# Kernel optimization log

Measured on AMD Instinct MI355X. Metric: run time of the kernel, lower is better.

The kernel has to match this reference:

```python
import jax, jax.numpy as jnp
import numpy as np

B, S, N = 8, 32, 64
F_NODE = 32
TRI = N * (N - 1) // 2        # 2016 upper-triangular edge features per step
DIN = F_NODE + TRI            # 2048 GATConv input dim (node feats + broadcast edge feats)
H, DOUT = 4, 256              # num_heads, hidden_channels
R = 1024                      # rnn_hidden_size
OUT = TRI                     # edge_in_channels * N*(N-1)/2


def setup_inputs() -> dict:
    key = jax.random.key(0)
    ks = jax.random.split(key, 16)
    def nrm(k, shape, fan):
        return jax.random.normal(k, shape, jnp.float32) / np.float32(np.sqrt(fan))
    # complete directed graph (no self loops; GATConv adds them)
    idx = np.arange(N)
    src = np.repeat(idx, N); dst = np.tile(idx, N)
    keep = src != dst
    edge_index = jnp.asarray(np.stack([src[keep], dst[keep]]), dtype=jnp.int32)  # [2, 4032]
    return {
        "x_node": jax.random.normal(ks[0], (B, S, N, F_NODE), jnp.float32),
        "x_edge": jax.random.normal(ks[1], (B, S, TRI), jnp.float32),
        "edge_index": edge_index,
        "W_gat": nrm(ks[2], (DIN, H * DOUT), DIN),
        "att_src": nrm(ks[3], (H, DOUT), DOUT),
        "att_dst": nrm(ks[4], (H, DOUT), DOUT),
        "b_gat": jnp.zeros((DOUT,), jnp.float32),
        "W_ih0": nrm(ks[5], (3 * R, N * DOUT), N * DOUT),
        "W_hh0": nrm(ks[6], (3 * R, R), R),
        "b_ih0": jnp.zeros((3 * R,), jnp.float32),
        "b_hh0": jnp.zeros((3 * R,), jnp.float32),
        "W_ih1": nrm(ks[7], (3 * R, R), R),
        "W_hh1": nrm(ks[8], (3 * R, R), R),
        "b_ih1": jnp.zeros((3 * R,), jnp.float32),
        "b_hh1": jnp.zeros((3 * R,), jnp.float32),
        "W_fc": nrm(ks[9], (R, OUT), R),
        "b_fc": jnp.zeros((OUT,), jnp.float32),
    }


def _gru_layer(x, Wih, Whh, bih, bhh):
    # x: [B, S, D] -> [B, S, R], PyTorch GRU equations
    def step(h, xt):
        gi = xt @ Wih.T + bih
        gh = h @ Whh.T + bhh
        i_r, i_z, i_n = jnp.split(gi, 3, axis=-1)
        h_r, h_z, h_n = jnp.split(gh, 3, axis=-1)
        r = jax.nn.sigmoid(i_r + h_r)
        z = jax.nn.sigmoid(i_z + h_z)
        n = jnp.tanh(i_n + r * h_n)
        h = (1.0 - z) * n + z * h
        return h, h
    h0 = jnp.zeros((x.shape[0], Whh.shape[1]), x.dtype)
    _, ys = jax.lax.scan(step, h0, jnp.swapaxes(x, 0, 1))
    return jnp.swapaxes(ys, 0, 1)


def reference(x_node, x_edge, edge_index, W_gat, att_src, att_dst, b_gat,
              W_ih0, W_hh0, b_ih0, b_hh0, W_ih1, W_hh1, b_ih1, b_hh1, W_fc, b_fc):
    # concat node feats with per-step edge features broadcast to every node
    x = jnp.concatenate(
        [x_node, jnp.broadcast_to(x_edge[:, :, None, :], (B, S, N, TRI))], axis=-1)
    xg = x.reshape(B * S, N, DIN)                         # batch all (b,t) graphs
    h = (xg @ W_gat).reshape(B * S, N, H, DOUT)           # per-head projections
    a_s = jnp.einsum('bnhe,he->bnh', h, att_src)
    a_d = jnp.einsum('bnhe,he->bnh', h, att_dst)
    # edge (src j -> dst i): leaky_relu(a_src[j] + a_dst[i]); dense over [dst, src]
    scores = jax.nn.leaky_relu(a_d[:, :, None, :] + a_s[:, None, :, :], 0.2)  # [BS, i, j, H]
    adj = jnp.zeros((N, N), bool).at[edge_index[1], edge_index[0]].set(True)
    adj = adj.at[jnp.arange(N), jnp.arange(N)].set(True)  # GATConv add_self_loops=True
    scores = jnp.where(adj[None, :, :, None], scores, -jnp.inf)
    alpha = jax.nn.softmax(scores, axis=2)                # softmax over source neighbors
    gat = jnp.einsum('bish,bshe->bihe', alpha, h).mean(axis=2) + b_gat  # concat=False -> head mean
    gat = jax.nn.relu(gat)                                # [BS, N, DOUT]
    seq = gat.reshape(B, S, N * DOUT)
    y = _gru_layer(seq, W_ih0, W_hh0, b_ih0, b_hh0)
    y = _gru_layer(y, W_ih1, W_hh1, b_ih1, b_hh1)
    return y[:, -1] @ W_fc + b_fc                         # [B, OUT]
```

## Files before the change

kernel.cpp:

```cpp
#include <hip/hip_runtime.h>
#include <hip/hip_bf16.h>

using bf16 = __hip_bfloat16;
typedef __bf16 bf16x8 __attribute__((ext_vector_type(8)));
typedef float f32x4 __attribute__((ext_vector_type(4)));


__device__ __forceinline__ void unp2(unsigned int u, float& a, float& b) {
  a = __uint_as_float(u << 16);
  b = __uint_as_float(u & 0xffff0000u);
}

__device__ __forceinline__ bf16x8 cvt8(float4 a, float4 b) {
  bf16x8 r;
  r[0] = (__bf16)a.x; r[1] = (__bf16)a.y; r[2] = (__bf16)a.z; r[3] = (__bf16)a.w;
  r[4] = (__bf16)b.x; r[5] = (__bf16)b.y; r[6] = (__bf16)b.z; r[7] = (__bf16)b.w;
  return r;
}

__global__ __launch_bounds__(256) void gru_fused_k(
    const float* __restrict__ X0,
    const float* __restrict__ Whh0,
    const float* __restrict__ bhh0,
    float* __restrict__ y0,
    const float* __restrict__ Wih1,
    const float* __restrict__ bih1,
    const float* __restrict__ Whh1,
    const float* __restrict__ bhh1,
    float* __restrict__ y1,
    int t) {
  __shared__ float sA[8][1024];
  __shared__ float sB[8][1024];
  const int tid = threadIdx.x;
  const int wv = tid >> 6, lane = tid & 63;

  if (blockIdx.x < 256) {
    if (t >= 32) return;
    const int s = t;
    if (s == 0) {
#pragma unroll
      for (int q = 0; q < 8; ++q) {
        int idx = q * 256 + tid;
        *(float4*)&sA[idx >> 8][(idx & 255) * 4] = make_float4(0.f, 0.f, 0.f, 0.f);
      }
    } else {
#pragma unroll
      for (int q = 0; q < 8; ++q) {
        int idx = q * 256 + tid;
        int b = idx >> 8, kf = (idx & 255) * 4;
        *(float4*)&sA[b][kf] =
            *(const float4*)&y0[(size_t)(b * 32 + s - 1) * 1024 + kf];
      }
    }
    __syncthreads();
    const int j = blockIdx.x * 4 + wv;
    const float* Wr = Whh0 + (size_t)j * 1024;
    const float* Wz = Whh0 + (size_t)(1024 + j) * 1024;
    const float* Wn = Whh0 + (size_t)(2048 + j) * 1024;
    float accR[8] = {}, accZ[8] = {}, accN[8] = {};
#pragma unroll
    for (int kk = 0; kk < 4; ++kk) {
      const int k = kk * 256 + lane * 4;
      float4 wr = *(const float4*)&Wr[k];
      float4 wz = *(const float4*)&Wz[k];
      float4 wn = *(const float4*)&Wn[k];
#pragma unroll
      for (int b = 0; b < 8; ++b) {
        float4 h4 = *(const float4*)&sA[b][k];
        accR[b] += h4.x * wr.x + h4.y * wr.y + h4.z * wr.z + h4.w * wr.w;
        accZ[b] += h4.x * wz.x + h4.y * wz.y + h4.z * wz.z + h4.w * wz.w;
        accN[b] += h4.x * wn.x + h4.y * wn.y + h4.z * wn.z + h4.w * wn.w;
      }
    }
#pragma unroll
    for (int d = 1; d < 64; d <<= 1) {
#pragma unroll
      for (int b = 0; b < 8; ++b) {
        accR[b] += __shfl_xor(accR[b], d);
        accZ[b] += __shfl_xor(accZ[b], d);
        accN[b] += __shfl_xor(accN[b], d);
      }
    }
    if (lane < 8) {
      const int b = lane;
      float sr = 0.f, sz = 0.f, sn = 0.f;
#pragma unroll
      for (int bb = 0; bb < 8; ++bb)
        if (b == bb) { sr = accR[bb]; sz = accZ[bb]; sn = accN[bb]; }
      const float* gip = X0 + (size_t)(b * 32 + s) * 3072;
      float r = 1.0f / (1.0f + __expf(-(gip[j] + sr + bhh0[j])));
      float z = 1.0f / (1.0f + __expf(-(gip[1024 + j] + sz + bhh0[1024 + j])));
      float n = tanhf(gip[2048 + j] + r * (sn + bhh0[2048 + j]));
      float hp = sA[b][j];
      y0[(size_t)(b * 32 + s) * 1024 + j] = (1.0f - z) * n + z * hp;
    }
  } else {
    if (t < 1) return;
    const int s = t - 1;
    {
#pragma unroll
      for (int q = 0; q < 8; ++q) {
        int idx = q * 256 + tid;
        int b = idx >> 8, kf = (idx & 255) * 4;
        *(float4*)&sA[b][kf] =
            *(const float4*)&y0[(size_t)(b * 32 + s) * 1024 + kf];
        float4 v = make_float4(0.f, 0.f, 0.f, 0.f);
        if (s > 0)
          v = *(const float4*)&y1[(size_t)(b * 32 + s - 1) * 1024 + kf];
        *(float4*)&sB[b][kf] = v;
      }
    }
    __syncthreads();
    const int j = (blockIdx.x - 256) * 4 + wv;
    const float* WiR = Wih1 + (size_t)j * 1024;
    const float* WiZ = Wih1 + (size_t)(1024 + j) * 1024;
    const float* WiN = Wih1 + (size_t)(2048 + j) * 1024;
    const float* WhR = Whh1 + (size_t)j * 1024;
    const float* WhZ = Whh1 + (size_t)(1024 + j) * 1024;
    const float* WhN = Whh1 + (size_t)(2048 + j) * 1024;
    float accRZ[8] = {}, accZZ[8] = {}, accIN[8] = {}, accHN[8] = {};
#pragma unroll
    for (int kk = 0; kk < 4; ++kk) {
      const int k = kk * 256 + lane * 4;
      float4 wir = *(const float4*)&WiR[k];
      float4 wiz = *(const float4*)&WiZ[k];
      float4 win = *(const float4*)&WiN[k];
      float4 whr = *(const float4*)&WhR[k];
      float4 whz = *(const float4*)&WhZ[k];
      float4 whn = *(const float4*)&WhN[k];
#pragma unroll
      for (int b = 0; b < 8; ++b) {
        float4 x4 = *(const float4*)&sA[b][k];
        float4 h4 = *(const float4*)&sB[b][k];
        accRZ[b] += x4.x * wir.x + x4.y * wir.y + x4.z * wir.z + x4.w * wir.w
                  + h4.x * whr.x + h4.y * whr.y + h4.z * whr.z + h4.w * whr.w;
        accZZ[b] += x4.x * wiz.x + x4.y * wiz.y + x4.z * wiz.z + x4.w * wiz.w
                  + h4.x * whz.x + h4.y * whz.y + h4.z * whz.z + h4.w * whz.w;
        accIN[b] += x4.x * win.x + x4.y * win.y + x4.z * win.z + x4.w * win.w;
        accHN[b] += h4.x * whn.x + h4.y * whn.y + h4.z * whn.z + h4.w * whn.w;
      }
    }
#pragma unroll
    for (int d = 1; d < 64; d <<= 1) {
#pragma unroll
      for (int b = 0; b < 8; ++b) {
        accRZ[b] += __shfl_xor(accRZ[b], d);
        accZZ[b] += __shfl_xor(accZZ[b], d);
        accIN[b] += __shfl_xor(accIN[b], d);
        accHN[b] += __shfl_xor(accHN[b], d);
      }
    }
    if (lane < 8) {
      const int b = lane;
      float srz = 0.f, szz = 0.f, sin_ = 0.f, shn = 0.f;
#pragma unroll
      for (int bb = 0; bb < 8; ++bb)
        if (b == bb) { srz = accRZ[bb]; szz = accZZ[bb]; sin_ = accIN[bb]; shn = accHN[bb]; }
      float r = 1.0f / (1.0f + __expf(-(srz + bih1[j] + bhh1[j])));
      float z = 1.0f / (1.0f + __expf(-(szz + bih1[1024 + j] + bhh1[1024 + j])));
      float n = tanhf(sin_ + bih1[2048 + j] + r * (shn + bhh1[2048 + j]));
      float hp = sB[b][j];
      y1[(size_t)(b * 32 + s) * 1024 + j] = (1.0f - z) * n + z * hp;
    }
  }
}

__global__ __launch_bounds__(256) void gemm_bt16_k(const __bf16* __restrict__ A,
                                                   const float* __restrict__ Bm,
                                                   float* __restrict__ Cp,
                                                   int N, int K, int ksper) {
  __shared__ __bf16 As[256][40];
  __shared__ __bf16 Bs[128][40];
  const int tid = threadIdx.x;
  const int bn = blockIdx.x * 128;
  const int lane = tid & 63, wv = tid >> 6;
  const int wr = wv >> 1, wc = wv & 1;
  const int lr = lane & 15, kh = lane >> 4;
  const int brow = tid >> 1, bhalf = tid & 1;
  f32x4 acc[8][4] = {};
  const int kstot = K >> 5;
  int ks0 = blockIdx.z * ksper;
  int ks1 = ks0 + ksper; if (ks1 > kstot) ks1 = kstot;
  uint4 ra0, ra1, ra2, ra3; float4 rb0, rb1, rb2, rb3;
  {
    const int k0 = ks0 << 5;
    const uint4* ap = (const uint4*)(A + (size_t)tid * K + k0);
    ra0 = ap[0]; ra1 = ap[1]; ra2 = ap[2]; ra3 = ap[3];
    const float* bp = Bm + (size_t)(bn + brow) * K + k0 + bhalf * 16;
    rb0 = ((const float4*)bp)[0]; rb1 = ((const float4*)bp)[1];
    rb2 = ((const float4*)bp)[2]; rb3 = ((const float4*)bp)[3];
  }
  for (int ks = ks0; ks < ks1; ++ks) {
    __syncthreads();
    *(uint4*)&As[tid][0]  = ra0;
    *(uint4*)&As[tid][8]  = ra1;
    *(uint4*)&As[tid][16] = ra2;
    *(uint4*)&As[tid][24] = ra3;
    *(bf16x8*)&Bs[brow][bhalf * 16] = cvt8(rb0, rb1);
    *(bf16x8*)&Bs[brow][bhalf * 16 + 8] = cvt8(rb2, rb3);
    __syncthreads();
    if (ks + 1 < ks1) {
      const int k0 = (ks + 1) << 5;
      const uint4* ap = (const uint4*)(A + (size_t)tid * K + k0);
      ra0 = ap[0]; ra1 = ap[1]; ra2 = ap[2]; ra3 = ap[3];
      const float* bp = Bm + (size_t)(bn + brow) * K + k0 + bhalf * 16;
      rb0 = ((const float4*)bp)[0]; rb1 = ((const float4*)bp)[1];
      rb2 = ((const float4*)bp)[2]; rb3 = ((const float4*)bp)[3];
    }
    bf16x8 bfv[4];
#pragma unroll
    for (int ni = 0; ni < 4; ++ni)
      bfv[ni] = *(const bf16x8*)&Bs[wc * 64 + ni * 16 + lr][kh * 8];
#pragma unroll
    for (int mi = 0; mi < 8; ++mi) {
      bf16x8 af = *(const bf16x8*)&As[wr * 128 + mi * 16 + lr][kh * 8];
#pragma unroll
      for (int ni = 0; ni < 4; ++ni)
        acc[mi][ni] = __builtin_amdgcn_mfma_f32_16x16x32_bf16(af, bfv[ni],
                                                              acc[mi][ni], 0, 0, 0);
    }
  }
  float* cp = Cp + (size_t)blockIdx.z * 256 * N;
#pragma unroll
  for (int mi = 0; mi < 8; ++mi) {
#pragma unroll
    for (int ni = 0; ni < 4; ++ni) {
      const int row = wr * 128 + mi * 16 + kh * 4;
      const int col = bn + wc * 64 + ni * 16 + lr;
#pragma unroll
      for (int j = 0; j < 4; ++j)
        cp[(size_t)(row + j) * N + col] = acc[mi][ni][j];
    }
  }
}

template <bool BT>
__global__ __launch_bounds__(256) void mfma_gemm_k(const float* __restrict__ A,
                                                   const float* __restrict__ Bm,
                                                   float* __restrict__ Cp,
                                                   int M, int N, int K,
                                                   int lda, int ldb, int ksper) {
  __shared__ __bf16 As[128][40];
  __shared__ __bf16 Bs[128][40];
  const int tid = threadIdx.x;
  const int bm = blockIdx.y * 128, bn = blockIdx.x * 128;
  const int lane = tid & 63, wv = tid >> 6;
  const int wr = wv >> 1, wc = wv & 1;
  const int lr = lane & 15, kh = lane >> 4;
  f32x4 acc[4][4] = {};
  const int kstot = K >> 5;
  int ks0 = blockIdx.z * ksper;
  int ks1 = ks0 + ksper; if (ks1 > kstot) ks1 = kstot;
  for (int ks = ks0; ks < ks1; ++ks) {
    const int k0 = ks << 5;
    __syncthreads();
    {
      const int row = tid >> 1, half = tid & 1;
      const float* ap = A + (size_t)(bm + row) * lda + k0 + half * 16;
      float4 f0 = ((const float4*)ap)[0], f1 = ((const float4*)ap)[1];
      float4 f2 = ((const float4*)ap)[2], f3 = ((const float4*)ap)[3];
      *(bf16x8*)&As[row][half * 16] = cvt8(f0, f1);
      *(bf16x8*)&As[row][half * 16 + 8] = cvt8(f2, f3);
    }
    if (BT) {
      const int row = tid >> 1, half = tid & 1;
      const float* bp = Bm + (size_t)(bn + row) * ldb + k0 + half * 16;
      float4 f0 = ((const float4*)bp)[0], f1 = ((const float4*)bp)[1];
      float4 f2 = ((const float4*)bp)[2], f3 = ((const float4*)bp)[3];
      *(bf16x8*)&Bs[row][half * 16] = cvt8(f0, f1);
      *(bf16x8*)&Bs[row][half * 16 + 8] = cvt8(f2, f3);
    } else {
      const int kk = tid >> 3, ng = tid & 7;
      const float* bp = Bm + (size_t)(k0 + kk) * ldb + bn + ng * 16;
      float4 f[4];
#pragma unroll
      for (int q = 0; q < 4; ++q) f[q] = ((const float4*)bp)[q];
#pragma unroll
      for (int q = 0; q < 4; ++q) {
        Bs[ng * 16 + q * 4 + 0][kk] = (__bf16)f[q].x;
        Bs[ng * 16 + q * 4 + 1][kk] = (__bf16)f[q].y;
        Bs[ng * 16 + q * 4 + 2][kk] = (__bf16)f[q].z;
        Bs[ng * 16 + q * 4 + 3][kk] = (__bf16)f[q].w;
      }
    }
    __syncthreads();
    bf16x8 af[4], bfv[4];
#pragma unroll
    for (int mi = 0; mi < 4; ++mi)
      af[mi] = *(const bf16x8*)&As[wr * 64 + mi * 16 + lr][kh * 8];
#pragma unroll
    for (int ni = 0; ni < 4; ++ni)
      bfv[ni] = *(const bf16x8*)&Bs[wc * 64 + ni * 16 + lr][kh * 8];
#pragma unroll
    for (int mi = 0; mi < 4; ++mi)
#pragma unroll
      for (int ni = 0; ni < 4; ++ni)
        acc[mi][ni] = __builtin_amdgcn_mfma_f32_16x16x32_bf16(af[mi], bfv[ni],
                                                              acc[mi][ni], 0, 0, 0);
  }
  float* cp = Cp + (size_t)blockIdx.z * M * N;
#pragma unroll
  for (int mi = 0; mi < 4; ++mi) {
#pragma unroll
    for (int ni = 0; ni < 4; ++ni) {
      const int row = bm + wr * 64 + mi * 16 + kh * 4;
      const int col = bn + wc * 64 + ni * 16 + lr;
#pragma unroll
      for (int j = 0; j < 4; ++j)
        cp[(size_t)(row + j) * N + col] = acc[mi][ni][j];
    }
  }
}

__global__ __launch_bounds__(256) void reduce_k(const float* __restrict__ Cp,
                                                const float* __restrict__ bias,
                                                float* __restrict__ C,
                                                int MN, int N, int nsk) {
  int i = (blockIdx.x * 256 + threadIdx.x) * 4;
  if (i >= MN) return;
  float4 s = make_float4(0.f, 0.f, 0.f, 0.f);
  if (bias) s = *(const float4*)&bias[i % N];
  for (int sk = 0; sk < nsk; ++sk) {
    float4 p = *(const float4*)&Cp[(size_t)sk * MN + i];
    s.x += p.x; s.y += p.y; s.z += p.z; s.w += p.w;
  }
  *(float4*)&C[i] = s;
}

__global__ __launch_bounds__(256) void node_h_k(const float* __restrict__ xn,
                                                const float* __restrict__ Wg,
                                                const float* __restrict__ he,
                                                bf16* __restrict__ hbuf) {
  __shared__ float xns[64][32];
  __shared__ float wgs[32][256];
  const int cq = blockIdx.x, g = blockIdx.y;
  const int tid = threadIdx.x;
  for (int idx = tid; idx < 2048; idx += 256) xns[idx >> 5][idx & 31] = xn[g * 2048 + idx];
  for (int r = 0; r < 32; ++r) wgs[r][tid] = Wg[r * 1024 + cq * 256 + tid];
  __syncthreads();
  const float hev = he[g * 1024 + cq * 256 + tid];
  for (int n0 = 0; n0 < 64; n0 += 8) {
    float acc[8];
#pragma unroll
    for (int nn = 0; nn < 8; ++nn) acc[nn] = hev;
    for (int f = 0; f < 32; ++f) {
      float w = wgs[f][tid];
#pragma unroll
      for (int nn = 0; nn < 8; ++nn) acc[nn] += xns[n0 + nn][f] * w;
    }
#pragma unroll
    for (int nn = 0; nn < 8; ++nn)
      hbuf[(size_t)(g * 64 + n0 + nn) * 1024 + cq * 256 + tid] = __float2bfloat16(acc[nn]);
  }
}

__global__ __launch_bounds__(256) void as_ad_k(const bf16* __restrict__ hbuf,
                                               const float* __restrict__ att_s,
                                               const float* __restrict__ att_d,
                                               float* __restrict__ as_o,
                                               float* __restrict__ ad_o) {
  const int tid = threadIdx.x;
  const int lane = tid & 63, wv = tid >> 6;
  const int row = blockIdx.x * 4 + wv;
  const int hd = lane >> 4;
  const int e0 = (lane & 15) * 16;
  float as_r[16], ad_r[16];
#pragma unroll
  for (int q = 0; q < 4; ++q) {
    float4 v = *(const float4*)(att_s + hd * 256 + e0 + q * 4);
    as_r[q * 4 + 0] = v.x; as_r[q * 4 + 1] = v.y; as_r[q * 4 + 2] = v.z; as_r[q * 4 + 3] = v.w;
    float4 w = *(const float4*)(att_d + hd * 256 + e0 + q * 4);
    ad_r[q * 4 + 0] = w.x; ad_r[q * 4 + 1] = w.y; ad_r[q * 4 + 2] = w.z; ad_r[q * 4 + 3] = w.w;
  }
  const uint4* hp = (const uint4*)(hbuf + (size_t)row * 1024 + lane * 16);
  uint4 p0 = hp[0], p1 = hp[1];
  float hv[16];
  unp2(p0.x, hv[0], hv[1]);  unp2(p0.y, hv[2], hv[3]);
  unp2(p0.z, hv[4], hv[5]);  unp2(p0.w, hv[6], hv[7]);
  unp2(p1.x, hv[8], hv[9]);  unp2(p1.y, hv[10], hv[11]);
  unp2(p1.z, hv[12], hv[13]); unp2(p1.w, hv[14], hv[15]);
  float ps = 0.f, pd = 0.f;
#pragma unroll
  for (int i = 0; i < 16; ++i) { ps += as_r[i] * hv[i]; pd += ad_r[i] * hv[i]; }
#pragma unroll
  for (int m = 1; m < 16; m <<= 1) { ps += __shfl_xor(ps, m); pd += __shfl_xor(pd, m); }
  if ((lane & 15) == 0) { as_o[row * 4 + hd] = ps; ad_o[row * 4 + hd] = pd; }
}

__global__ __launch_bounds__(256) void attn_agg_k(const bf16* __restrict__ hbuf,
                                                  const float* __restrict__ as_i,
                                                  const float* __restrict__ ad_i,
                                                  const float* __restrict__ bgat,
                                                  __bf16* __restrict__ seq) {
  __shared__ float ass[256], ads[256], bgs[256];
  __shared__ float alpha[4][64][64];
  __shared__ float hq[64][260];
  const int g = blockIdx.x, tid = threadIdx.x;
  ass[tid] = as_i[g * 256 + tid];
  ads[tid] = ad_i[g * 256 + tid];
  bgs[tid] = bgat[tid];
  __syncthreads();
  {
    const int hd = tid >> 6, i = tid & 63;
    const float ad = ads[i * 4 + hd];
    float m = -1e30f;
    for (int j = 0; j < 64; ++j) {
      float s = ad + ass[j * 4 + hd];
      s = s > 0.0f ? s : 0.2f * s;
      m = fmaxf(m, s);
    }
    float sum = 0.0f;
    for (int j = 0; j < 64; ++j) {
      float s = ad + ass[j * 4 + hd];
      s = s > 0.0f ? s : 0.2f * s;
      sum += __expf(s - m);
    }
    const float inv = 1.0f / sum;
    for (int j = 0; j < 64; ++j) {
      float s = ad + ass[j * 4 + hd];
      s = s > 0.0f ? s : 0.2f * s;
      alpha[hd][j][i] = __expf(s - m) * inv;
    }
  }
  const int i = tid & 63, eq = tid >> 6;
  float acc[64] = {};
  for (int hd = 0; hd < 4; ++hd) {
    __syncthreads();
    for (int idx = tid; idx < 2048; idx += 256) {
      int j = idx >> 5, ch = idx & 31;
      uint4 p = *(const uint4*)(hbuf + (size_t)(g * 64 + j) * 1024 + hd * 256 + ch * 8);
      float f0, f1, f2, f3, f4, f5, f6, f7;
      unp2(p.x, f0, f1); unp2(p.y, f2, f3); unp2(p.z, f4, f5); unp2(p.w, f6, f7);
      *(float4*)&hq[j][ch * 8] = make_float4(f0, f1, f2, f3);
      *(float4*)&hq[j][ch * 8 + 4] = make_float4(f4, f5, f6, f7);
    }
    __syncthreads();
    for (int j = 0; j < 64; ++j) {
      const float a = alpha[hd][j][i];
      const float* hr = &hq[j][eq * 64];
#pragma unroll
      for (int q = 0; q < 16; ++q) {
        float4 hv = *(const float4*)(hr + q * 4);
        acc[q * 4 + 0] += a * hv.x; acc[q * 4 + 1] += a * hv.y;
        acc[q * 4 + 2] += a * hv.z; acc[q * 4 + 3] += a * hv.w;
      }
    }
  }
  __bf16* op = seq + (size_t)g * 16384 + i * 256 + eq * 64;
#pragma unroll
  for (int q = 0; q < 8; ++q) {
    float4 lo, hi;
    lo.x = fmaxf(bgs[eq * 64 + q * 8 + 0] + 0.25f * acc[q * 8 + 0], 0.0f);
    lo.y = fmaxf(bgs[eq * 64 + q * 8 + 1] + 0.25f * acc[q * 8 + 1], 0.0f);
    lo.z = fmaxf(bgs[eq * 64 + q * 8 + 2] + 0.25f * acc[q * 8 + 2], 0.0f);
    lo.w = fmaxf(bgs[eq * 64 + q * 8 + 3] + 0.25f * acc[q * 8 + 3], 0.0f);
    hi.x = fmaxf(bgs[eq * 64 + q * 8 + 4] + 0.25f * acc[q * 8 + 4], 0.0f);
    hi.y = fmaxf(bgs[eq * 64 + q * 8 + 5] + 0.25f * acc[q * 8 + 5], 0.0f);
    hi.z = fmaxf(bgs[eq * 64 + q * 8 + 6] + 0.25f * acc[q * 8 + 6], 0.0f);
    hi.w = fmaxf(bgs[eq * 64 + q * 8 + 7] + 0.25f * acc[q * 8 + 7], 0.0f);
    *(bf16x8*)(op + q * 8) = cvt8(lo, hi);
  }
}

__global__ __launch_bounds__(256) void fc_k(const float* __restrict__ y1,
                                            const float* __restrict__ Wfc,
                                            const float* __restrict__ bfc,
                                            float* __restrict__ out) {
  __shared__ float As[8][1024];
  const int tid = threadIdx.x;
  for (int idx = tid; idx < 8192; idx += 256) {
    int b = idx >> 10, k = idx & 1023;
    As[b][k] = y1[(size_t)(b * 32 + 31) * 1024 + k];
  }
  __syncthreads();
  const int ol = tid >> 2, kq = tid & 3;
  const int o = blockIdx.x * 64 + ol;
  float acc[8] = {};
  if (o < 2016) {
    for (int i2 = 0; i2 < 256; ++i2) {
      int k = i2 * 4 + kq;
      float w = Wfc[(size_t)k * 2016 + o];
#pragma unroll
      for (int b = 0; b < 8; ++b) acc[b] += As[b][k] * w;
    }
  }
#pragma unroll
  for (int b = 0; b < 8; ++b) {
    acc[b] += __shfl_xor(acc[b], 1);
    acc[b] += __shfl_xor(acc[b], 2);
  }
  if (kq == 0 && o < 2016) {
#pragma unroll
    for (int b = 0; b < 8; ++b) out[b * 2016 + o] = acc[b] + bfc[o];
  }
}

extern "C" void kernel_launch(void* const* d_in, const int* in_sizes, int n_in,
                              void* d_out, int out_size, void* d_ws, size_t ws_size,
                              hipStream_t stream) {
  (void)in_sizes; (void)n_in; (void)out_size; (void)ws_size;
  const float* x_node = (const float*)d_in[0];
  const float* x_edge = (const float*)d_in[1];
  const float* W_gat = (const float*)d_in[3];
  const float* att_s = (const float*)d_in[4];
  const float* att_d = (const float*)d_in[5];
  const float* b_gat = (const float*)d_in[6];
  const float* W_ih0 = (const float*)d_in[7];
  const float* W_hh0 = (const float*)d_in[8];
  const float* b_ih0 = (const float*)d_in[9];
  const float* b_hh0 = (const float*)d_in[10];
  const float* W_ih1 = (const float*)d_in[11];
  const float* W_hh1 = (const float*)d_in[12];
  const float* b_ih1 = (const float*)d_in[13];
  const float* b_hh1 = (const float*)d_in[14];
  const float* W_fc  = (const float*)d_in[15];
  const float* b_fc  = (const float*)d_in[16];

  char* ws = (char*)d_ws;
  size_t off = 0;
  float*  he  = (float*)(ws + off);  off += 256u * 1024 * 4;
  float*  a_s = (float*)(ws + off);  off += 256u * 64 * 4 * 4;
  float*  a_d = (float*)(ws + off);  off += 256u * 64 * 4 * 4;
  bf16*   hb  = (bf16*)(ws + off);   off += 256u * 64 * 1024 * 2;
  __bf16* seq = (__bf16*)(ws + off); off += 256u * 16384 * 2;
  float*  X0  = (float*)(ws + off);  off += 256u * 3072 * 4;
  float*  y0  = (float*)(ws + off);  off += 256u * 1024 * 4;
  float*  y1  = (float*)(ws + off);  off += 256u * 1024 * 4;
  off = (off + 255) & ~(size_t)255;
  float*  Cp  = (float*)(ws + off);  off += (size_t)16 * 256 * 3072 * 4;

  mfma_gemm_k<false><<<dim3(8, 2, 8), 256, 0, stream>>>(
      x_edge, W_gat + 32 * 1024, Cp, 256, 1024, 2016, 2016, 1024, 8);
  reduce_k<<<256, 256, 0, stream>>>(Cp, nullptr, he, 256 * 1024, 1024, 8);
  node_h_k<<<dim3(4, 256), 256, 0, stream>>>(x_node, W_gat, he, hb);
  as_ad_k<<<4096, 256, 0, stream>>>(hb, att_s, att_d, a_s, a_d);
  attn_agg_k<<<256, 256, 0, stream>>>(hb, a_s, a_d, b_gat, seq);
  gemm_bt16_k<<<dim3(24, 1, 16), 256, 0, stream>>>(seq, W_ih0, Cp,
                                                   3072, 16384, 32);
  reduce_k<<<768, 256, 0, stream>>>(Cp, b_ih0, X0, 256 * 3072, 3072, 16);
  for (int t = 0; t <= 32; ++t)
    gru_fused_k<<<512, 256, 0, stream>>>(X0, W_hh0, b_hh0, y0,
                                         W_ih1, b_ih1, W_hh1, b_hh1, y1, t);
  fc_k<<<32, 256, 0, stream>>>(y1, W_fc, b_fc, (float*)d_out);
}
```

Baseline: 765.4 us.

## Store GRU recurrent weights in bf16 and split layer-1 work across more blocks

Adds a kernel that converts W_hh0, W_ih1 and W_hh1 to bf16 once per call, which halves the weight bytes each GRU step streams from memory. The layer-1 part of the fused GRU kernel now runs on twice as many blocks. Each block handles two output units, with separate waves for the input and hidden projections, and their partial sums are combined through shared memory. This raises parallelism for the weight-bandwidth-bound recurrent steps. In exchange it adds a conversion pass over 3x3M weights, lowers weight precision, and reads the previous h directly from global memory instead of staging it in LDS.

```diff
diff --git a/kernel.cpp b/kernel.cpp
--- a/kernel.cpp
+++ b/kernel.cpp
@@ -18,19 +18,34 @@
   return r;
 }
 
-__global__ __launch_bounds__(256) void gru_fused_k(
+__global__ __launch_bounds__(256) void wcvt_k(const float* __restrict__ a,
+                                              const float* __restrict__ b,
+                                              const float* __restrict__ c,
+                                              __bf16* __restrict__ A,
+                                              __bf16* __restrict__ B,
+                                              __bf16* __restrict__ C) {
+  const int i = (blockIdx.x * 256 + threadIdx.x) * 8;
+  float4 x0 = *(const float4*)&a[i], x1 = *(const float4*)&a[i + 4];
+  *(bf16x8*)&A[i] = cvt8(x0, x1);
+  float4 y0_ = *(const float4*)&b[i], y1_ = *(const float4*)&b[i + 4];
+  *(bf16x8*)&B[i] = cvt8(y0_, y1_);
+  float4 z0 = *(const float4*)&c[i], z1 = *(const float4*)&c[i + 4];
+  *(bf16x8*)&C[i] = cvt8(z0, z1);
+}
+
+__global__ __launch_bounds__(256) void gru_fused2_k(
     const float* __restrict__ X0,
-    const float* __restrict__ Whh0,
+    const __bf16* __restrict__ Wb0,
     const float* __restrict__ bhh0,
     float* __restrict__ y0,
-    const float* __restrict__ Wih1,
+    const __bf16* __restrict__ Wbi1,
     const float* __restrict__ bih1,
-    const float* __restrict__ Whh1,
+    const __bf16* __restrict__ Wbh1,
     const float* __restrict__ bhh1,
     float* __restrict__ y1,
     int t) {
   __shared__ float sA[8][1024];
-  __shared__ float sB[8][1024];
+  __shared__ float part[2][2][3][8];
   const int tid = threadIdx.x;
   const int wv = tid >> 6, lane = tid & 63;
 
@@ -54,22 +69,26 @@
     }
     __syncthreads();
     const int j = blockIdx.x * 4 + wv;
-    const float* Wr = Whh0 + (size_t)j * 1024;
-    const float* Wz = Whh0 + (size_t)(1024 + j) * 1024;
-    const float* Wn = Whh0 + (size_t)(2048 + j) * 1024;
+    const __bf16* Wr = Wb0 + (size_t)j * 1024;
+    const __bf16* Wz = Wb0 + (size_t)(1024 + j) * 1024;
+    const __bf16* Wn = Wb0 + (size_t)(2048 + j) * 1024;
     float accR[8] = {}, accZ[8] = {}, accN[8] = {};
 #pragma unroll
     for (int kk = 0; kk < 4; ++kk) {
       const int k = kk * 256 + lane * 4;
-      float4 wr = *(const float4*)&Wr[k];
-      float4 wz = *(const float4*)&Wz[k];
-      float4 wn = *(const float4*)&Wn[k];
+      uint2 uR = *(const uint2*)&Wr[k];
+      uint2 uZ = *(const uint2*)&Wz[k];
+      uint2 uN = *(const uint2*)&Wn[k];
+      float r0, r1, r2, r3, z0, z1, z2, z3, n0, n1, n2, n3;
+      unp2(uR.x, r0, r1); unp2(uR.y, r2, r3);
+      unp2(uZ.x, z0, z1); unp2(uZ.y, z2, z3);
+      unp2(uN.x, n0, n1); unp2(uN.y, n2, n3);
 #pragma unroll
       for (int b = 0; b < 8; ++b) {
         float4 h4 = *(const float4*)&sA[b][k];
-        accR[b] += h4.x * wr.x + h4.y * wr.y + h4.z * wr.z + h4.w * wr.w;
-        accZ[b] += h4.x * wz.x + h4.y * wz.y + h4.z * wz.z + h4.w * wz.w;
-        accN[b] += h4.x * wn.x + h4.y * wn.y + h4.z * wn.z + h4.w * wn.w;
+        accR[b] += h4.x * r0 + h4.y * r1 + h4.z * r2 + h4.w * r3;
+        accZ[b] += h4.x * z0 + h4.y * z1 + h4.z * z2 + h4.w * z3;
+        accN[b] += h4.x * n0 + h4.y * n1 + h4.z * n2 + h4.w * n3;
       }
     }
 #pragma unroll
@@ -97,69 +116,75 @@
   } else {
     if (t < 1) return;
     const int s = t - 1;
-    {
-#pragma unroll
-      for (int q = 0; q < 8; ++q) {
-        int idx = q * 256 + tid;
-        int b = idx >> 8, kf = (idx & 255) * 4;
-        *(float4*)&sA[b][kf] =
-            *(const float4*)&y0[(size_t)(b * 32 + s) * 1024 + kf];
-        float4 v = make_float4(0.f, 0.f, 0.f, 0.f);
-        if (s > 0)
-          v = *(const float4*)&y1[(size_t)(b * 32 + s - 1) * 1024 + kf];
-        *(float4*)&sB[b][kf] = v;
-      }
-    }
-    __syncthreads();
-    const int j = (blockIdx.x - 256) * 4 + wv;
-    const float* WiR = Wih1 + (size_t)j * 1024;
-    const float* WiZ = Wih1 + (size_t)(1024 + j) * 1024;
-    const float* WiN = Wih1 + (size_t)(2048 + j) * 1024;
-    const float* WhR = Whh1 + (size_t)j * 1024;
-    const float* WhZ = Whh1 + (size_t)(1024 + j) * 1024;
-    const float* WhN = Whh1 + (size_t)(2048 + j) * 1024;
-    float accRZ[8] = {}, accZZ[8] = {}, accIN[8] = {}, accHN[8] = {};
+#pragma unroll
+    for (int q = 0; q < 8; ++q) {
+      int idx = q * 256 + tid;
+      int b = idx >> 8, kf = (idx & 255) * 4;
+      *(float4*)&sA[b][kf] =
+          *(const float4*)&y0[(size_t)(b * 32 + s) * 1024 + kf];
+    }
+    __syncthreads();
+    const int jb = (int)(blockIdx.x - 256) * 2;
+    const int p = wv >> 1, role = wv & 1;
+    const int j = jb + p;
+    const __bf16* Wm = role ? Wbh1 : Wbi1;
+    const __bf16* WR = Wm + (size_t)j * 1024;
+    const __bf16* WZ = Wm + (size_t)(1024 + j) * 1024;
+    const __bf16* WN = Wm + (size_t)(2048 + j) * 1024;
+    float aR[8] = {}, aZ[8] = {}, aN[8] = {};
 #pragma unroll
     for (int kk = 0; kk < 4; ++kk) {
       const int k = kk * 256 + lane * 4;
-      float4 wir = *(const float4*)&WiR[k];
-      float4 wiz = *(const float4*)&WiZ[k];
-      float4 win = *(const float4*)&WiN[k];
-      float4 whr = *(const float4*)&WhR[k];
-      float4 whz = *(const float4*)&WhZ[k];
-      float4 whn = *(const float4*)&WhN[k];
+      uint2 uR = *(const uint2*)&WR[k];
+      uint2 uZ = *(const uint2*)&WZ[k];
+      uint2 uN = *(const uint2*)&WN[k];
+      float r0, r1, r2, r3, z0, z1, z2, z3, n0, n1, n2, n3;
+      unp2(uR.x, r0, r1); unp2(uR.y, r2, r3);
+      unp2(uZ.x, z0, z1); unp2(uZ.y, z2, z3);
+      unp2(uN.x, n0, n1); unp2(uN.y, n2, n3);
 #pragma unroll
       for (int b = 0; b < 8; ++b) {
-        float4 x4 = *(const float4*)&sA[b][k];
-        float4 h4 = *(const float4*)&sB[b][k];
-        accRZ[b] += x4.x * wir.x + x4.y * wir.y + x4.z * wir.z + x4.w * wir.w
-                  + h4.x * whr.x + h4.y * whr.y + h4.z * whr.z + h4.w * whr.w;
-        accZZ[b] += x4.x * wiz.x + x4.y * wiz.y + x4.z * wiz.z + x4.w * wiz.w
-                  + h4.x * whz.x + h4.y * whz.y + h4.z * whz.z + h4.w * whz.w;
-        accIN[b] += x4.x * win.x + x4.y * win.y + x4.z * win.z + x4.w * win.w;
-        accHN[b] += h4.x * whn.x + h4.y * whn.y + h4.z * whn.z + h4.w * whn.w;
+        float4 v;
+        if (role) {
+          if (s > 0)
+            v = *(const float4*)&y1[(size_t)(b * 32 + s - 1) * 1024 + k];
+          else
+            v = make_float4(0.f, 0.f, 0.f, 0.f);
+        } else {
+          v = *(const float4*)&sA[b][k];
+        }
+        aR[b] += v.x * r0 + v.y * r1 + v.z * r2 + v.w * r3;
+        aZ[b] += v.x * z0 + v.y * z1 + v.z * z2 + v.w * z3;
+        aN[b] += v.x * n0 + v.y * n1 + v.z * n2 + v.w * n3;
       }
     }
 #pragma unroll
     for (int d = 1; d < 64; d <<= 1) {
 #pragma unroll
       for (int b = 0; b < 8; ++b) {
-        accRZ[b] += __shfl_xor(accRZ[b], d);
-        accZZ[b] += __shfl_xor(accZZ[b], d);
-        accIN[b] += __shfl_xor(accIN[b], d);
-        accHN[b] += __shfl_xor(accHN[b], d);
-      }
-    }
-    if (lane < 8) {
+        aR[b] += __shfl_xor(aR[b], d);
+        aZ[b] += __shfl_xor(aZ[b], d);
+        aN[b] += __shfl_xor(aN[b], d);
+      }
+    }
+    if (lane == 0) {
+#pragma unroll
+      for (int b = 0; b < 8; ++b) {
+        part[p][role][0][b] = aR[b];
+        part[p][role][1][b] = aZ[b];
+        part[p][role][2][b] = aN[b];
+      }
+    }
+    __syncthreads();
+    if (role == 0 && lane < 8) {
       const int b = lane;
-      float srz = 0.f, szz = 0.f, sin_ = 0.f, shn = 0.f;
-#pragma unroll
-      for (int bb = 0; bb < 8; ++bb)
-        if (b == bb) { srz = accRZ[bb]; szz = accZZ[bb]; sin_ = accIN[bb]; shn = accHN[bb]; }
-      float r = 1.0f / (1.0f + __expf(-(srz + bih1[j] + bhh1[j])));
-      float z = 1.0f / (1.0f + __expf(-(szz + bih1[1024 + j] + bhh1[1024 + j])));
-      float n = tanhf(sin_ + bih1[2048 + j] + r * (shn + bhh1[2048 + j]));
-      float hp = sB[b][j];
+      float xR = part[p][0][0][b], hR = part[p][1][0][b];
+      float xZ = part[p][0][1][b], hZ = part[p][1][1][b];
+      float xN = part[p][0][2][b], hN = part[p][1][2][b];
+      float r = 1.0f / (1.0f + __expf(-(xR + hR + bih1[j] + bhh1[j])));
+      float z = 1.0f / (1.0f + __expf(-(xZ + hZ + bih1[1024 + j] + bhh1[1024 + j])));
+      float n = tanhf(xN + bih1[2048 + j] + r * (hN + bhh1[2048 + j]));
+      float hp = (s > 0) ? y1[(size_t)(b * 32 + s - 1) * 1024 + j] : 0.f;
       y1[(size_t)(b * 32 + s) * 1024 + j] = (1.0f - z) * n + z * hp;
     }
   }
@@ -518,17 +543,21 @@
 
   char* ws = (char*)d_ws;
   size_t off = 0;
-  float*  he  = (float*)(ws + off);  off += 256u * 1024 * 4;
-  float*  a_s = (float*)(ws + off);  off += 256u * 64 * 4 * 4;
-  float*  a_d = (float*)(ws + off);  off += 256u * 64 * 4 * 4;
-  bf16*   hb  = (bf16*)(ws + off);   off += 256u * 64 * 1024 * 2;
-  __bf16* seq = (__bf16*)(ws + off); off += 256u * 16384 * 2;
-  float*  X0  = (float*)(ws + off);  off += 256u * 3072 * 4;
-  float*  y0  = (float*)(ws + off);  off += 256u * 1024 * 4;
-  float*  y1  = (float*)(ws + off);  off += 256u * 1024 * 4;
+  float*  he   = (float*)(ws + off);   off += 256u * 1024 * 4;
+  float*  a_s  = (float*)(ws + off);   off += 256u * 64 * 4 * 4;
+  float*  a_d  = (float*)(ws + off);   off += 256u * 64 * 4 * 4;
+  bf16*   hb   = (bf16*)(ws + off);    off += 256u * 64 * 1024 * 2;
+  __bf16* seq  = (__bf16*)(ws + off);  off += 256u * 16384 * 2;
+  float*  X0   = (float*)(ws + off);   off += 256u * 3072 * 4;
+  float*  y0   = (float*)(ws + off);   off += 256u * 1024 * 4;
+  float*  y1   = (float*)(ws + off);   off += 256u * 1024 * 4;
+  __bf16* Wb0  = (__bf16*)(ws + off);  off += 3072u * 1024 * 2;
+  __bf16* Wbi1 = (__bf16*)(ws + off);  off += 3072u * 1024 * 2;
+  __bf16* Wbh1 = (__bf16*)(ws + off);  off += 3072u * 1024 * 2;
   off = (off + 255) & ~(size_t)255;
-  float*  Cp  = (float*)(ws + off);  off += (size_t)16 * 256 * 3072 * 4;
-
+  float*  Cp   = (float*)(ws + off);   off += (size_t)16 * 256 * 3072 * 4;
+
+  wcvt_k<<<1536, 256, 0, stream>>>(W_hh0, W_ih1, W_hh1, Wb0, Wbi1, Wbh1);
   mfma_gemm_k<false><<<dim3(8, 2, 8), 256, 0, stream>>>(
       x_edge, W_gat + 32 * 1024, Cp, 256, 1024, 2016, 2016, 1024, 8);
   reduce_k<<<256, 256, 0, stream>>>(Cp, nullptr, he, 256 * 1024, 1024, 8);
@@ -539,7 +568,7 @@
                                                    3072, 16384, 32);
   reduce_k<<<768, 256, 0, stream>>>(Cp, b_ih0, X0, 256 * 3072, 3072, 16);
   for (int t = 0; t <= 32; ++t)
-    gru_fused_k<<<512, 256, 0, stream>>>(X0, W_hh0, b_hh0, y0,
-                                         W_ih1, b_ih1, W_hh1, b_hh1, y1, t);
+    gru_fused2_k<<<768, 256, 0, stream>>>(X0, Wb0, b_hh0, y0,
+                                          Wbi1, b_ih1, Wbh1, b_hh1, y1, t);
   fc_k<<<32, 256, 0, stream>>>(y1, W_fc, b_fc, (float*)d_out);
 }
```

New measurement: 655.2 us (median of 2 runs). 14.4% less time.
